# Kernel optimization log

Hardware: AMD Instinct MI355X
Metric: run time of the kernel (lower is better)

The kernel has to match this reference:

```python
import jax, jax.numpy as jnp
import numpy as np

N = 4096   # num nodes
D = 512    # hidden_dim
H = 8      # head_num (hardcoded in module)
E = 131072 # num relation pairs
DH = D // H


def setup_inputs() -> dict:
    key = jax.random.key(0)
    k1, k2, k3, k4, k5, k6 = jax.random.split(key, 6)
    inst_feature = jax.random.normal(k1, (N, D), jnp.float32)
    aggregator_matrix = jax.random.randint(k2, (N, N), 0, 2).astype(jnp.float32)
    # unique (sub, obj) pairs to avoid nondeterministic duplicate scatter-set
    rng = np.random.default_rng(0)
    flat = rng.choice(N * N, size=E, replace=False)
    rel_pair_index = jnp.stack(
        [jnp.asarray(flat // N, jnp.int32), jnp.asarray(flat % N, jnp.int32)], axis=1)
    std = np.sqrt(2.0 / (D + DH)).astype(np.float32)
    w_q = jax.random.normal(k3, (D, D), jnp.float32) * std
    w_k = jax.random.normal(k4, (D, D), jnp.float32) * std
    bnd = 1.0 / np.sqrt(D)
    b_q = jax.random.uniform(k5, (D,), jnp.float32, -bnd, bnd)
    b_k = jax.random.uniform(k6, (D,), jnp.float32, -bnd, bnd)
    return {"inst_feature": inst_feature, "aggregator_matrix": aggregator_matrix,
            "rel_pair_index": rel_pair_index, "w_q": w_q, "b_q": b_q,
            "w_k": w_k, "b_k": b_k}


def reference(inst_feature, aggregator_matrix, rel_pair_index, w_q, b_q, w_k, b_k):
    n, d = inst_feature.shape
    sub = rel_pair_index[:, 0]
    obj = rel_pair_index[:, 1]
    # gather + project (eval mode: dropouts are identity)
    q = (inst_feature[sub] @ w_q.T + b_q).reshape(-1, H, DH)  # [E,H,dh]
    k = (inst_feature[obj] @ w_k.T + b_k).reshape(-1, H, DH)  # [E,H,dh]
    scores = (q * k).sum(-1) / np.sqrt(DH).astype(np.float32)  # [E,H]
    # scatter into dense [H,N,N]
    af = jnp.zeros((H, n, n), inst_feature.dtype).at[:, sub, obj].set(scores.T)
    # mask where aggregator_matrix == 0 (applied before diagonal override)
    af = jnp.where((aggregator_matrix == 0)[None], -jnp.inf, af)
    diag = jnp.arange(n)
    af = af.at[:, diag, diag].set(1e-7)
    p = jax.nn.softmax(af, axis=2)          # softmax over last dim
    factor = p.sum(axis=0) / H              # [N,N]
    return factor @ inst_feature            # [N,D]
```

## Files before the change

kernel.cpp:

```cpp
#include <hip/hip_runtime.h>

#define N_INST 4096
#define D_FEAT 512
#define NHEAD 8
#define NPAIR 131072

typedef __attribute__((ext_vector_type(8))) short short8;
typedef __attribute__((ext_vector_type(4))) float f32x4;
typedef __attribute__((ext_vector_type(4))) unsigned short u16x4;

__device__ inline unsigned short f2bf(float f) {
  union { float f; unsigned u; } v; v.f = f;
  unsigned r = v.u + 0x7fffu + ((v.u >> 16) & 1u);
  return (unsigned short)(r >> 16);
}
__device__ inline float bf2f(unsigned short b) {
  union { unsigned u; float f; } v; v.u = ((unsigned)b) << 16; return v.f;
}
__device__ inline void gload16(const void* g, void* l) {
  __builtin_amdgcn_global_load_lds((const __attribute__((address_space(1))) unsigned int*)g,
                                   (__attribute__((address_space(3))) unsigned int*)l, 16, 0, 0);
}

__global__ __launch_bounds__(256) void k_castw(const float* __restrict__ wq,
                                               const float* __restrict__ wk,
                                               unsigned short* __restrict__ dst) {
  const float* src = blockIdx.y ? wk : wq;
  unsigned short* d = dst + (size_t)blockIdx.y * D_FEAT * D_FEAT;
  int i = (blockIdx.x * 256 + threadIdx.x) * 4;
  float4 v = *(const float4*)&src[i];
  ushort4 o;
  o.x = f2bf(v.x); o.y = f2bf(v.y); o.z = f2bf(v.z); o.w = f2bf(v.w);
  *(ushort4*)&d[i] = o;
}

__global__ __launch_bounds__(256) void k_xprep(const float* __restrict__ x,
                                               unsigned short* __restrict__ xb,
                                               unsigned short* __restrict__ xT) {
  __shared__ float t[32][33];
  int bx = blockIdx.x, by = blockIdx.y;
  int tx = threadIdx.x & 31, ty = threadIdx.x >> 5;
  #pragma unroll
  for (int r = 0; r < 4; ++r) {
    int row = by * 32 + ty + r * 8;
    float v = x[(size_t)row * D_FEAT + bx * 32 + tx];
    t[ty + r * 8][tx] = v;
    xb[(size_t)row * D_FEAT + bx * 32 + tx] = f2bf(v);
  }
  __syncthreads();
  #pragma unroll
  for (int r = 0; r < 4; ++r)
    xT[(size_t)(bx * 32 + ty + r * 8) * N_INST + by * 32 + tx] = f2bf(t[tx][ty + r * 8]);
}

__global__ __launch_bounds__(256) void k_mask_acnt(const float* __restrict__ agg,
                                                   unsigned short* __restrict__ maskb,
                                                   int* __restrict__ acnt,
                                                   unsigned char* __restrict__ vbits) {
  int i0 = blockIdx.x * 2;
  const f32x4* r0 = (const f32x4*)(agg + (size_t)i0 * N_INST);
  const f32x4* r1 = (const f32x4*)(agg + (size_t)(i0 + 1) * N_INST);
  u16x4* m0 = (u16x4*)(maskb + (size_t)i0 * N_INST);
  u16x4* m1 = (u16x4*)(maskb + (size_t)(i0 + 1) * N_INST);
  unsigned char* v0r = vbits + (size_t)i0 * (N_INST / 4);
  unsigned char* v1r = vbits + (size_t)(i0 + 1) * (N_INST / 4);
  int tid = threadIdx.x;
  f32x4 v[8];
  #pragma unroll
  for (int u = 0; u < 4; ++u) {
    v[u]     = __builtin_nontemporal_load(&r0[u * 256 + tid]);
    v[4 + u] = __builtin_nontemporal_load(&r1[u * 256 + tid]);
  }
  int cnt0 = 0, cnt1 = 0;
  #pragma unroll
  for (int u = 0; u < 4; ++u) {
    int t = u * 256 + tid;
    int j = t * 4;
    {
      f32x4 w = v[u];
      int b0 = (w[0] != 0.f), b1 = (w[1] != 0.f), b2 = (w[2] != 0.f), b3 = (w[3] != 0.f);
      u16x4 m;
      m[0] = b0 ? 0x3F80 : 0; m[1] = b1 ? 0x3F80 : 0;
      m[2] = b2 ? 0x3F80 : 0; m[3] = b3 ? 0x3F80 : 0;
      cnt0 += b0 + b1 + b2 + b3;
      v0r[t] = (unsigned char)(b0 | (b1 << 1) | (b2 << 2) | (b3 << 3));
      if (i0 >= j && i0 < j + 4) {
        int d = i0 - j;
        m[d] = 0x3F80;
        cnt0 -= (w[d] != 0.f);
      }
      __builtin_nontemporal_store(m, &m0[t]);
    }
    {
      f32x4 w = v[4 + u];
      int i1 = i0 + 1;
      int b0 = (w[0] != 0.f), b1 = (w[1] != 0.f), b2 = (w[2] != 0.f), b3 = (w[3] != 0.f);
      u16x4 m;
      m[0] = b0 ? 0x3F80 : 0; m[1] = b1 ? 0x3F80 : 0;
      m[2] = b2 ? 0x3F80 : 0; m[3] = b3 ? 0x3F80 : 0;
      cnt1 += b0 + b1 + b2 + b3;
      v1r[t] = (unsigned char)(b0 | (b1 << 1) | (b2 << 2) | (b3 << 3));
      if (i1 >= j && i1 < j + 4) {
        int d = i1 - j;
        m[d] = 0x3F80;
        cnt1 -= (w[d] != 0.f);
      }
      __builtin_nontemporal_store(m, &m1[t]);
    }
  }
  #pragma unroll
  for (int msk = 1; msk < 64; msk <<= 1) {
    cnt0 += __shfl_xor(cnt0, msk);
    cnt1 += __shfl_xor(cnt1, msk);
  }
  __shared__ int wsum[4][2];
  if ((threadIdx.x & 63) == 0) {
    wsum[threadIdx.x >> 6][0] = cnt0;
    wsum[threadIdx.x >> 6][1] = cnt1;
  }
  __syncthreads();
  if (threadIdx.x == 0)
    acnt[i0] = wsum[0][0] + wsum[1][0] + wsum[2][0] + wsum[3][0];
  if (threadIdx.x == 1)
    acnt[i0 + 1] = wsum[0][1] + wsum[1][1] + wsum[2][1] + wsum[3][1];
}

template<int BIAS, int CBF16, int BN>
__global__ __launch_bounds__(256, 2) void k_gemm(const unsigned short* __restrict__ A,
                                                 const unsigned short* __restrict__ B,
                                                 const float* __restrict__ bias0,
                                                 const float* __restrict__ bias1,
                                                 void* __restrict__ Cv,
                                                 int M, int N, int K, int klen) {
  constexpr int NI = BN / 32;
  constexpr int BCH = BN / 32;
  __shared__ __align__(16) unsigned short lA[2][128 * 64];
  __shared__ __align__(16) unsigned short lB[2][BN * 64];
  int tid = threadIdx.x, wave = tid >> 6, lane = tid & 63;
  int wm = wave & 1, wn = wave >> 1;
  int gx = gridDim.x;
  int nxy = gx * gridDim.y;
  int lin = blockIdx.x + gx * blockIdx.y;
  int nch = nxy >> 3;
  int nl = (lin & 7) * nch + (lin >> 3);
  int bx = nl % gx, by = nl / gx;
  int bm = by * 128, bn = bx * BN;
  int kbase = blockIdx.z * klen;
  int srow = lane >> 3;
  int sg = (lane & 7) ^ srow;
  const unsigned short* ag[4];
  const unsigned short* bg[BCH];
  #pragma unroll
  for (int p = 0; p < 4; ++p) {
    int row = (wave * 4 + p) * 8 + srow;
    ag[p] = A + (size_t)(bm + row) * K + kbase + sg * 8;
  }
  #pragma unroll
  for (int p = 0; p < BCH; ++p) {
    int row = (wave * BCH + p) * 8 + srow;
    bg[p] = B + (size_t)(bn + row) * K + kbase + sg * 8;
  }
  auto stage = [&](int buf) {
    #pragma unroll
    for (int p = 0; p < 4; ++p) { gload16(ag[p], &lA[buf][(wave * 4 + p) * 512]); ag[p] += 64; }
    #pragma unroll
    for (int p = 0; p < BCH; ++p) { gload16(bg[p], &lB[buf][(wave * BCH + p) * 512]); bg[p] += 64; }
  };
  f32x4 acc[4][NI] = {};
  int nt = klen / 64;
  stage(0);
  __syncthreads();
  int cur = 0;
  int lrow = lane & 15, glq = lane >> 4;
  for (int t = 0; t < nt; ++t) {
    if (t + 1 < nt) stage(cur ^ 1);
    short8 bf[2][NI];
    #pragma unroll
    for (int kk = 0; kk < 2; ++kk)
      #pragma unroll
      for (int ni = 0; ni < NI; ++ni) {
        int row = wn * (BN / 2) + ni * 16 + lrow;
        int pg = (kk * 4 + glq) ^ (row & 7);
        bf[kk][ni] = *(const short8*)&lB[cur][row * 64 + pg * 8];
      }
    #pragma unroll
    for (int mi = 0; mi < 4; ++mi)
      #pragma unroll
      for (int kk = 0; kk < 2; ++kk) {
        int row = wm * 64 + mi * 16 + lrow;
        int pg = (kk * 4 + glq) ^ (row & 7);
        short8 af = *(const short8*)&lA[cur][row * 64 + pg * 8];
        #pragma unroll
        for (int ni = 0; ni < NI; ++ni)
          acc[mi][ni] = __builtin_amdgcn_mfma_f32_16x16x32_bf16(af, bf[kk][ni], acc[mi][ni], 0, 0, 0);
      }
    __syncthreads();
    cur ^= 1;
  }
  #pragma unroll
  for (int mi = 0; mi < 4; ++mi)
    #pragma unroll
    for (int ni = 0; ni < NI; ++ni) {
      int col = bn + wn * (BN / 2) + ni * 16 + lrow;
      float bv = 0.f;
      if (BIAS) bv = (col < 512) ? bias0[col] : bias1[col - 512];
      #pragma unroll
      for (int j = 0; j < 4; ++j) {
        int row = bm + wm * 64 + mi * 16 + glq * 4 + j;
        float vv = acc[mi][ni][j] + bv;
        if (CBF16) {
          unsigned short* C = (unsigned short*)Cv + (size_t)blockIdx.z * M * N;
          C[(size_t)row * N + col] = f2bf(vv);
        } else {
          float* C = (float*)Cv + (size_t)blockIdx.z * M * N;
          C[(size_t)row * N + col] = vv;
        }
      }
    }
}

__global__ __launch_bounds__(256) void k_scores(const unsigned short* __restrict__ QKb,
                                                const int* __restrict__ pairs,
                                                const unsigned char* __restrict__ vbits,
                                                float* __restrict__ es,
                                                float* __restrict__ sumexp,
                                                int* __restrict__ scnt) {
  int wave = threadIdx.x >> 6, lane = threadIdx.x & 63;
  int half = lane >> 5, hl = lane & 31;
  int e = (blockIdx.x * 4 + wave) * 2 + half;
  int2 pr = *(const int2*)&pairs[2 * e];
  int sub = pr.x, obj = pr.y;
  unsigned char nb = vbits[(size_t)sub * (N_INST / 4) + (obj >> 2)];
  bool valid = (sub != obj) && ((nb >> (obj & 3)) & 1);
  if (!valid && hl == 0) es[(size_t)e * 8] = -1.f;
  if (__ballot(valid) == 0ull) return;
  float pa = 0.f, pb = 0.f;
  if (valid) {
    short8 qa = *(const short8*)&QKb[(size_t)sub * 1024 + hl * 8];
    short8 qb = *(const short8*)&QKb[(size_t)sub * 1024 + 256 + hl * 8];
    short8 ka = *(const short8*)&QKb[(size_t)obj * 1024 + 512 + hl * 8];
    short8 kb = *(const short8*)&QKb[(size_t)obj * 1024 + 768 + hl * 8];
    #pragma unroll
    for (int j = 0; j < 8; ++j) {
      pa += bf2f((unsigned short)qa[j]) * bf2f((unsigned short)ka[j]);
      pb += bf2f((unsigned short)qb[j]) * bf2f((unsigned short)kb[j]);
    }
  }
  pa += __shfl_xor(pa, 1); pa += __shfl_xor(pa, 2); pa += __shfl_xor(pa, 4);
  pb += __shfl_xor(pb, 1); pb += __shfl_xor(pb, 2); pb += __shfl_xor(pb, 4);
  if (valid && (hl & 7) == 0) {
    int g = hl >> 3;
    float ea = expf(pa * 0.125f);
    float eb = expf(pb * 0.125f);
    es[(size_t)e * 8 + g] = ea;
    es[(size_t)e * 8 + 4 + g] = eb;
    atomicAdd(&sumexp[sub * 8 + g], ea);
    atomicAdd(&sumexp[sub * 8 + 4 + g], eb);
    if (g == 0) atomicAdd(&scnt[sub], 1);
  }
}

__global__ __launch_bounds__(256) void k_denom(const float* __restrict__ sumexp,
                                               const int* __restrict__ scnt,
                                               const int* __restrict__ acnt,
                                               float* __restrict__ invden,
                                               float* __restrict__ base) {
  int i = blockIdx.x * 256 + threadIdx.x;
  if (i >= N_INST) return;
  float c0 = (float)(acnt[i] - scnt[i]);
  const float E0 = expf(1e-7f);
  float bsum = 0.f;
  #pragma unroll
  for (int h = 0; h < NHEAD; ++h) {
    float inv = 1.0f / (E0 + c0 + sumexp[i * NHEAD + h]);
    invden[i * NHEAD + h] = inv;
    bsum += inv;
  }
  base[i] = bsum * (1.0f / NHEAD);
}

__global__ __launch_bounds__(256) void k_scatter(const int* __restrict__ pairs,
                                                 const float* __restrict__ es,
                                                 const float* __restrict__ invden,
                                                 const float* __restrict__ base,
                                                 unsigned short* __restrict__ maskb) {
  int e = blockIdx.x * 256 + threadIdx.x;
  if (e >= NPAIR) return;
  float4 e0 = *(const float4*)&es[(size_t)e * 8];
  if (e0.x < 0.f) return;
  float4 e1 = *(const float4*)&es[(size_t)e * 8 + 4];
  int sub = pairs[2 * e], obj = pairs[2 * e + 1];
  const float* inv = &invden[sub * 8];
  float f = e0.x * inv[0] + e0.y * inv[1] + e0.z * inv[2] + e0.w * inv[3] +
            e1.x * inv[4] + e1.y * inv[5] + e1.z * inv[6] + e1.w * inv[7];
  maskb[(size_t)sub * N_INST + obj] = f2bf(f * 0.125f / base[sub]);
}

__global__ __launch_bounds__(256) void k_redscale(const unsigned short* __restrict__ P,
                                                  const float* __restrict__ base,
                                                  float* __restrict__ out) {
  size_t idx = ((size_t)blockIdx.x * 256 + threadIdx.x) * 4;
  int i = (int)(idx >> 9);
  const size_t S = (size_t)N_INST * 512;
  u16x4 a = *(const u16x4*)&P[idx];
  u16x4 b = *(const u16x4*)&P[idx + S];
  u16x4 c = *(const u16x4*)&P[idx + 2 * S];
  u16x4 d = *(const u16x4*)&P[idx + 3 * S];
  float s = base[i];
  float4 o;
  o.x = s * (bf2f(a[0]) + bf2f(b[0]) + bf2f(c[0]) + bf2f(d[0]));
  o.y = s * (bf2f(a[1]) + bf2f(b[1]) + bf2f(c[1]) + bf2f(d[1]));
  o.z = s * (bf2f(a[2]) + bf2f(b[2]) + bf2f(c[2]) + bf2f(d[2]));
  o.w = s * (bf2f(a[3]) + bf2f(b[3]) + bf2f(c[3]) + bf2f(d[3]));
  *(float4*)&out[idx] = o;
}

extern "C" void kernel_launch(void* const* d_in, const int* in_sizes, int n_in,
                              void* d_out, int out_size, void* d_ws, size_t ws_size,
                              hipStream_t stream) {
  const float* x   = (const float*)d_in[0];
  const float* agg = (const float*)d_in[1];
  const int*   prs = (const int*)d_in[2];
  const float* w_q = (const float*)d_in[3];
  const float* b_q = (const float*)d_in[4];
  const float* w_k = (const float*)d_in[5];
  const float* b_k = (const float*)d_in[6];
  float* out = (float*)d_out;

  char* ws = (char*)d_ws;
  size_t off = 0;
  auto alloc = [&](size_t bytes) -> void* {
    void* p = ws + off;
    off += (bytes + 255) & ~(size_t)255;
    return p;
  };
  unsigned short* xb    = (unsigned short*)alloc((size_t)N_INST * D_FEAT * 2);
  unsigned short* xbT   = (unsigned short*)alloc((size_t)D_FEAT * N_INST * 2);
  unsigned short* wqkb  = (unsigned short*)alloc((size_t)1024 * D_FEAT * 2);
  void*           QKP   = alloc((size_t)N_INST * 512 * 2 * 4);
  float*          es    = (float*)alloc((size_t)NPAIR * NHEAD * 4);
  float*          sumexp= (float*)alloc((size_t)N_INST * NHEAD * 4);
  int*            scnt  = (int*)alloc((size_t)N_INST * 4);
  int*            acnt  = (int*)alloc((size_t)N_INST * 4);
  float*          invden= (float*)alloc((size_t)N_INST * NHEAD * 4);
  float*          base  = (float*)alloc((size_t)N_INST * 4);
  unsigned char*  vbits = (unsigned char*)alloc((size_t)N_INST * (N_INST / 4));
  unsigned short* maskb = (unsigned short*)alloc((size_t)N_INST * N_INST * 2);

  hipMemsetAsync(sumexp, 0, (size_t)N_INST * NHEAD * 4, stream);
  hipMemsetAsync(scnt, 0, (size_t)N_INST * 4, stream);

  k_castw<<<dim3(D_FEAT * D_FEAT / 4 / 256, 2), 256, 0, stream>>>(w_q, w_k, wqkb);
  k_xprep<<<dim3(D_FEAT / 32, N_INST / 32), 256, 0, stream>>>(x, xb, xbT);
  k_mask_acnt<<<dim3(N_INST / 2), 256, 0, stream>>>(agg, maskb, acnt, vbits);

  k_gemm<1, 1, 64><<<dim3(1024 / 64, N_INST / 128, 1), 256, 0, stream>>>(
      xb, wqkb, b_q, b_k, QKP, N_INST, 1024, D_FEAT, D_FEAT);

  k_scores<<<dim3(NPAIR / 8), 256, 0, stream>>>((const unsigned short*)QKP, prs, vbits, es, sumexp, scnt);
  k_denom<<<dim3(N_INST / 256), 256, 0, stream>>>(sumexp, scnt, acnt, invden, base);
  k_scatter<<<dim3(NPAIR / 256), 256, 0, stream>>>(prs, es, invden, base, maskb);

  k_gemm<0, 1, 128><<<dim3(512 / 128, N_INST / 128, 4), 256, 0, stream>>>(
      maskb, xbT, nullptr, nullptr, QKP, N_INST, 512, N_INST, N_INST / 4);

  k_redscale<<<dim3(N_INST * 512 / 4 / 256), 256, 0, stream>>>((const unsigned short*)QKP, base, out);
}
```

Baseline: 107.5 us.

## Single-buffer split-K 8 aggregation GEMM, widen scores and reduce kernels

The final aggregation GEMM now uses split-K of 8 with a single LDS buffer and launch bounds allowing 4 blocks per CU, which doubles the grid and raises occupancy in exchange for losing the load/compute overlap. The scores kernel now handles four pairs per wave with 16 lanes each and four head-pair chunks per lane. The reduce kernel sums eight bf16 partials with 8-wide loads. The two memsets are merged into one, relying on scnt sitting right after sumexp in the workspace. The price is more partial-buffer traffic and more bf16 rounding of partial sums.

```diff
diff --git a/kernel.cpp b/kernel.cpp
--- a/kernel.cpp
+++ b/kernel.cpp
@@ -4,10 +4,12 @@
 #define D_FEAT 512
 #define NHEAD 8
 #define NPAIR 131072
+#define SPLITK 8
 
 typedef __attribute__((ext_vector_type(8))) short short8;
 typedef __attribute__((ext_vector_type(4))) float f32x4;
 typedef __attribute__((ext_vector_type(4))) unsigned short u16x4;
+typedef __attribute__((ext_vector_type(8))) unsigned short u16x8;
 
 __device__ inline unsigned short f2bf(float f) {
   union { float f; unsigned u; } v; v.f = f;
@@ -125,17 +127,18 @@
     acnt[i0 + 1] = wsum[0][1] + wsum[1][1] + wsum[2][1] + wsum[3][1];
 }
 
-template<int BIAS, int CBF16, int BN>
-__global__ __launch_bounds__(256, 2) void k_gemm(const unsigned short* __restrict__ A,
-                                                 const unsigned short* __restrict__ B,
-                                                 const float* __restrict__ bias0,
-                                                 const float* __restrict__ bias1,
-                                                 void* __restrict__ Cv,
-                                                 int M, int N, int K, int klen) {
+template<int BIAS, int CBF16, int BN, int NB>
+__global__ __launch_bounds__(256, NB == 1 ? 4 : 2) void k_gemm(
+    const unsigned short* __restrict__ A,
+    const unsigned short* __restrict__ B,
+    const float* __restrict__ bias0,
+    const float* __restrict__ bias1,
+    void* __restrict__ Cv,
+    int M, int N, int K, int klen) {
   constexpr int NI = BN / 32;
   constexpr int BCH = BN / 32;
-  __shared__ __align__(16) unsigned short lA[2][128 * 64];
-  __shared__ __align__(16) unsigned short lB[2][BN * 64];
+  __shared__ __align__(16) unsigned short lA[NB][128 * 64];
+  __shared__ __align__(16) unsigned short lB[NB][BN * 64];
   int tid = threadIdx.x, wave = tid >> 6, lane = tid & 63;
   int wm = wave & 1, wn = wave >> 1;
   int gx = gridDim.x;
@@ -168,12 +171,16 @@
   };
   f32x4 acc[4][NI] = {};
   int nt = klen / 64;
-  stage(0);
-  __syncthreads();
+  if (NB == 2) { stage(0); __syncthreads(); }
   int cur = 0;
   int lrow = lane & 15, glq = lane >> 4;
   for (int t = 0; t < nt; ++t) {
-    if (t + 1 < nt) stage(cur ^ 1);
+    if (NB == 2) {
+      if (t + 1 < nt) stage(cur ^ 1);
+    } else {
+      stage(0);
+      __syncthreads();
+    }
     short8 bf[2][NI];
     #pragma unroll
     for (int kk = 0; kk < 2; ++kk)
@@ -195,7 +202,7 @@
           acc[mi][ni] = __builtin_amdgcn_mfma_f32_16x16x32_bf16(af, bf[kk][ni], acc[mi][ni], 0, 0, 0);
       }
     __syncthreads();
-    cur ^= 1;
+    if (NB == 2) cur ^= 1;
   }
   #pragma unroll
   for (int mi = 0; mi < 4; ++mi)
@@ -226,37 +233,44 @@
                                                 float* __restrict__ sumexp,
                                                 int* __restrict__ scnt) {
   int wave = threadIdx.x >> 6, lane = threadIdx.x & 63;
-  int half = lane >> 5, hl = lane & 31;
-  int e = (blockIdx.x * 4 + wave) * 2 + half;
+  int q = lane >> 4, ql = lane & 15;
+  int e = (blockIdx.x * 4 + wave) * 4 + q;
   int2 pr = *(const int2*)&pairs[2 * e];
   int sub = pr.x, obj = pr.y;
   unsigned char nb = vbits[(size_t)sub * (N_INST / 4) + (obj >> 2)];
   bool valid = (sub != obj) && ((nb >> (obj & 3)) & 1);
-  if (!valid && hl == 0) es[(size_t)e * 8] = -1.f;
+  if (!valid && ql == 0) es[(size_t)e * 8] = -1.f;
   if (__ballot(valid) == 0ull) return;
-  float pa = 0.f, pb = 0.f;
+  float p[4] = {0.f, 0.f, 0.f, 0.f};
   if (valid) {
-    short8 qa = *(const short8*)&QKb[(size_t)sub * 1024 + hl * 8];
-    short8 qb = *(const short8*)&QKb[(size_t)sub * 1024 + 256 + hl * 8];
-    short8 ka = *(const short8*)&QKb[(size_t)obj * 1024 + 512 + hl * 8];
-    short8 kb = *(const short8*)&QKb[(size_t)obj * 1024 + 768 + hl * 8];
-    #pragma unroll
-    for (int j = 0; j < 8; ++j) {
-      pa += bf2f((unsigned short)qa[j]) * bf2f((unsigned short)ka[j]);
-      pb += bf2f((unsigned short)qb[j]) * bf2f((unsigned short)kb[j]);
-    }
-  }
-  pa += __shfl_xor(pa, 1); pa += __shfl_xor(pa, 2); pa += __shfl_xor(pa, 4);
-  pb += __shfl_xor(pb, 1); pb += __shfl_xor(pb, 2); pb += __shfl_xor(pb, 4);
-  if (valid && (hl & 7) == 0) {
-    int g = hl >> 3;
-    float ea = expf(pa * 0.125f);
-    float eb = expf(pb * 0.125f);
-    es[(size_t)e * 8 + g] = ea;
-    es[(size_t)e * 8 + 4 + g] = eb;
-    atomicAdd(&sumexp[sub * 8 + g], ea);
-    atomicAdd(&sumexp[sub * 8 + 4 + g], eb);
-    if (g == 0) atomicAdd(&scnt[sub], 1);
+    short8 qv[4], kv[4];
+    #pragma unroll
+    for (int c = 0; c < 4; ++c) {
+      qv[c] = *(const short8*)&QKb[(size_t)sub * 1024 + c * 128 + ql * 8];
+      kv[c] = *(const short8*)&QKb[(size_t)obj * 1024 + 512 + c * 128 + ql * 8];
+    }
+    #pragma unroll
+    for (int c = 0; c < 4; ++c)
+      #pragma unroll
+      for (int j = 0; j < 8; ++j)
+        p[c] += bf2f((unsigned short)qv[c][j]) * bf2f((unsigned short)kv[c][j]);
+  }
+  #pragma unroll
+  for (int c = 0; c < 4; ++c) {
+    p[c] += __shfl_xor(p[c], 1);
+    p[c] += __shfl_xor(p[c], 2);
+    p[c] += __shfl_xor(p[c], 4);
+  }
+  if (valid && (ql & 7) == 0) {
+    int hi = ql >> 3;
+    #pragma unroll
+    for (int c = 0; c < 4; ++c) {
+      int h = 2 * c + hi;
+      float ev = expf(p[c] * 0.125f);
+      es[(size_t)e * 8 + h] = ev;
+      atomicAdd(&sumexp[sub * 8 + h], ev);
+    }
+    if (ql == 0) atomicAdd(&scnt[sub], 1);
   }
 }
 
@@ -299,20 +313,28 @@
 __global__ __launch_bounds__(256) void k_redscale(const unsigned short* __restrict__ P,
                                                   const float* __restrict__ base,
                                                   float* __restrict__ out) {
-  size_t idx = ((size_t)blockIdx.x * 256 + threadIdx.x) * 4;
+  size_t idx = ((size_t)blockIdx.x * 256 + threadIdx.x) * 8;
   int i = (int)(idx >> 9);
   const size_t S = (size_t)N_INST * 512;
-  u16x4 a = *(const u16x4*)&P[idx];
-  u16x4 b = *(const u16x4*)&P[idx + S];
-  u16x4 c = *(const u16x4*)&P[idx + 2 * S];
-  u16x4 d = *(const u16x4*)&P[idx + 3 * S];
+  u16x8 v[SPLITK];
+  #pragma unroll
+  for (int z = 0; z < SPLITK; ++z)
+    v[z] = *(const u16x8*)&P[idx + z * S];
   float s = base[i];
-  float4 o;
-  o.x = s * (bf2f(a[0]) + bf2f(b[0]) + bf2f(c[0]) + bf2f(d[0]));
-  o.y = s * (bf2f(a[1]) + bf2f(b[1]) + bf2f(c[1]) + bf2f(d[1]));
-  o.z = s * (bf2f(a[2]) + bf2f(b[2]) + bf2f(c[2]) + bf2f(d[2]));
-  o.w = s * (bf2f(a[3]) + bf2f(b[3]) + bf2f(c[3]) + bf2f(d[3]));
-  *(float4*)&out[idx] = o;
+  float4 o0, o1;
+  #pragma unroll
+  for (int j = 0; j < 4; ++j) {
+    float a = 0.f, b = 0.f;
+    #pragma unroll
+    for (int z = 0; z < SPLITK; ++z) {
+      a += bf2f(v[z][j]);
+      b += bf2f(v[z][4 + j]);
+    }
+    ((float*)&o0)[j] = s * a;
+    ((float*)&o1)[j] = s * b;
+  }
+  *(float4*)&out[idx] = o0;
+  *(float4*)&out[idx + 4] = o1;
 }
 
 extern "C" void kernel_launch(void* const* d_in, const int* in_sizes, int n_in,
@@ -337,7 +359,7 @@
   unsigned short* xb    = (unsigned short*)alloc((size_t)N_INST * D_FEAT * 2);
   unsigned short* xbT   = (unsigned short*)alloc((size_t)D_FEAT * N_INST * 2);
   unsigned short* wqkb  = (unsigned short*)alloc((size_t)1024 * D_FEAT * 2);
-  void*           QKP   = alloc((size_t)N_INST * 512 * 2 * 4);
+  void*           QKP   = alloc((size_t)N_INST * 512 * 2 * SPLITK);
   float*          es    = (float*)alloc((size_t)NPAIR * NHEAD * 4);
   float*          sumexp= (float*)alloc((size_t)N_INST * NHEAD * 4);
   int*            scnt  = (int*)alloc((size_t)N_INST * 4);
@@ -347,22 +369,21 @@
   unsigned char*  vbits = (unsigned char*)alloc((size_t)N_INST * (N_INST / 4));
   unsigned short* maskb = (unsigned short*)alloc((size_t)N_INST * N_INST * 2);
 
-  hipMemsetAsync(sumexp, 0, (size_t)N_INST * NHEAD * 4, stream);
-  hipMemsetAsync(scnt, 0, (size_t)N_INST * 4, stream);
+  hipMemsetAsync(sumexp, 0, (size_t)N_INST * NHEAD * 4 + (size_t)N_INST * 4, stream);
 
   k_castw<<<dim3(D_FEAT * D_FEAT / 4 / 256, 2), 256, 0, stream>>>(w_q, w_k, wqkb);
   k_xprep<<<dim3(D_FEAT / 32, N_INST / 32), 256, 0, stream>>>(x, xb, xbT);
   k_mask_acnt<<<dim3(N_INST / 2), 256, 0, stream>>>(agg, maskb, acnt, vbits);
 
-  k_gemm<1, 1, 64><<<dim3(1024 / 64, N_INST / 128, 1), 256, 0, stream>>>(
+  k_gemm<1, 1, 64, 2><<<dim3(1024 / 64, N_INST / 128, 1), 256, 0, stream>>>(
       xb, wqkb, b_q, b_k, QKP, N_INST, 1024, D_FEAT, D_FEAT);
 
-  k_scores<<<dim3(NPAIR / 8), 256, 0, stream>>>((const unsigned short*)QKP, prs, vbits, es, sumexp, scnt);
+  k_scores<<<dim3(NPAIR / 16), 256, 0, stream>>>((const unsigned short*)QKP, prs, vbits, es, sumexp, scnt);
   k_denom<<<dim3(N_INST / 256), 256, 0, stream>>>(sumexp, scnt, acnt, invden, base);
   k_scatter<<<dim3(NPAIR / 256), 256, 0, stream>>>(prs, es, invden, base, maskb);
 
-  k_gemm<0, 1, 128><<<dim3(512 / 128, N_INST / 128, 4), 256, 0, stream>>>(
-      maskb, xbT, nullptr, nullptr, QKP, N_INST, 512, N_INST, N_INST / 4);
-
-  k_redscale<<<dim3(N_INST * 512 / 4 / 256), 256, 0, stream>>>((const unsigned short*)QKP, base, out);
-}
+  k_gemm<0, 1, 128, 1><<<dim3(512 / 128, N_INST / 128, SPLITK), 256, 0, stream>>>(
+      maskb, xbT, nullptr, nullptr, QKP, N_INST, 512, N_INST, N_INST / SPLITK);
+
+  k_redscale<<<dim3(N_INST * 512 / 8 / 256), 256, 0, stream>>>((const unsigned short*)QKP, base, out);
+}
```

New measurement: 113.7 us. +5.8%, slower.
